# Kernel optimization log

Hardware: AMD Instinct MI355X
Metric: run time of the kernel (lower is better)

The kernel has to match this reference:

```python
import jax, jax.numpy as jnp
import numpy as np

HIDDEN = 300
DEPTH = 3
MAX_NB = 10
AFEAT = 82
BFEAT = 6
B, N, M = 16, 2048, 4096


def setup_inputs() -> dict:
    key = jax.random.key(0)
    ks = jax.random.split(key, 16)
    s = 0.05
    return {
        "input_atom": jax.random.normal(ks[0], (B, N, AFEAT), jnp.float32),
        "input_bond": jax.random.normal(ks[1], (B, M, BFEAT), jnp.float32),
        "node_mask": jnp.ones((B, N, 1), jnp.float32),
        "atom_graph": jax.random.randint(ks[2], (B, N, MAX_NB), 0, N, jnp.int32),
        "bond_graph": jax.random.randint(ks[3], (B, N, MAX_NB), 0, M, jnp.int32),
        "num_nbs": jax.random.randint(ks[4], (B, N), 0, MAX_NB, jnp.int32),
        "W_af": jax.random.normal(ks[5], (AFEAT, HIDDEN), jnp.float32) * s,
        "W_na": jax.random.normal(ks[6], (HIDDEN, HIDDEN), jnp.float32) * s,
        "W_nb": jax.random.normal(ks[7], (BFEAT, HIDDEN), jnp.float32) * s,
        "W_sa": jax.random.normal(ks[8], (HIDDEN, HIDDEN), jnp.float32) * s,
        "W_u2": jax.random.normal(ks[9], (HIDDEN + BFEAT, HIDDEN), jnp.float32) * s,
        "b_u2": jnp.zeros((HIDDEN,), jnp.float32),
        "W_u1": jax.random.normal(ks[10], (2 * HIDDEN, HIDDEN), jnp.float32) * s,
        "b_u1": jnp.zeros((HIDDEN,), jnp.float32),
        "W_out": jax.random.normal(ks[11], (HIDDEN, 1), jnp.float32) * s,
        "b_out": jnp.zeros((1,), jnp.float32),
    }


def _wln(input_atom, input_bond, node_mask, atom_graph, bond_graph, num_nbs,
         W_af, W_na, W_nb, W_sa, W_u2, b_u2, W_u1, b_u1):
    bidx = jnp.arange(input_atom.shape[0])[:, None, None]  # (B,1,1)
    atom_feat = jax.nn.relu(input_atom @ W_af)             # (B,N,H)
    fbond_nei = input_bond[bidx, bond_graph]               # (B,N,max_nb,6) gather
    h_nei_bond = fbond_nei @ W_nb                          # constant over depth
    # neighbor validity mask from num_nbs (sequence mask)
    nb_mask = (jnp.arange(MAX_NB)[None, None, :] < num_nbs[..., None]
               ).astype(atom_feat.dtype)[..., None]        # (B,N,max_nb,1)
    kernel = None
    for _ in range(DEPTH):
        fatom_nei = atom_feat[bidx, atom_graph]            # (B,N,max_nb,H) gather
        h_nei = (fatom_nei @ W_na) * h_nei_bond
        f_nei = jnp.sum(h_nei * nb_mask, axis=-2)          # (B,N,H)
        f_self = atom_feat @ W_sa
        kernel = f_nei * f_self * node_mask                # last-layer WLN kernel
        l_nei = jnp.concatenate([fatom_nei, fbond_nei], axis=-1)
        pre_label = jax.nn.relu(l_nei @ W_u2 + b_u2)
        nei_label = jnp.sum(pre_label * nb_mask, axis=-2)
        new_label = jnp.concatenate([atom_feat, nei_label], axis=-1)
        atom_feat = jax.nn.relu(new_label @ W_u1 + b_u1)
    return kernel


def reference(input_atom, input_bond, node_mask, atom_graph, bond_graph, num_nbs,
              W_af, W_na, W_nb, W_sa, W_u2, b_u2, W_u1, b_u1, W_out, b_out):
    x = _wln(input_atom, input_bond, node_mask, atom_graph, bond_graph, num_nbs,
             W_af, W_na, W_nb, W_sa, W_u2, b_u2, W_u1, b_u1)  # (B,N,H)
    x = jnp.sum(x, axis=-2)                                   # sum pooling -> (B,H)
    return x @ W_out + b_out                                  # (B,1)
```

## Files before the change

kernel.cpp:

```cpp
#include <hip/hip_runtime.h>
#include <math.h>


typedef unsigned short ushort_t;
typedef __attribute__((ext_vector_type(8))) short bf16x8;
typedef __attribute__((ext_vector_type(8))) unsigned short ushort8;
typedef __attribute__((ext_vector_type(4))) float f32x4;

static constexpr int Hh  = 300;
static constexpr int Hp  = 320;
static constexpr int Bn  = 16;
static constexpr int Nn  = 2048;
static constexpr int Rn  = Bn * Nn;
static constexpr int NBn = 10;

static constexpr size_t OFF_U2 = 320 * 96;
static constexpr size_t OFF_NA = OFF_U2 + 320 * 320;
static constexpr size_t OFF_SA = OFF_NA + 320 * 320;
static constexpr size_t OFF_U1 = OFF_SA + 320 * 320;
static constexpr int    W_ELEMS = (int)(OFF_U1 + 320 * 640);

__device__ __forceinline__ ushort_t f2bf(float x) {
    union { float f; unsigned u; } c; c.f = x;
    unsigned r = c.u + 0x7FFFu + ((c.u >> 16) & 1u);
    return (ushort_t)(r >> 16);
}
__device__ __forceinline__ float bf2f(ushort_t h) {
    union { float f; unsigned u; } c; c.u = ((unsigned)h) << 16;
    return c.f;
}

template<bool RELU, bool BIAS, bool CONCAT>
__global__ __launch_bounds__(256)
void mfma_gemm_k(const ushort_t* __restrict__ A, const ushort_t* __restrict__ A2,
                 int lda, int KP,
                 const ushort_t* __restrict__ Wt,
                 const float* __restrict__ bias,
                 ushort_t* __restrict__ C)
{
    __shared__ __attribute__((aligned(16))) ushort_t As[256 * 40];
    __shared__ __attribute__((aligned(16))) ushort_t Bs[64 * 40];

    const int t   = threadIdx.x;
    const int wv  = t >> 6;
    const int ln  = t & 63;
    const int lrow = ln & 15;
    const int lgrp = ln >> 4;
    const int rowBase = blockIdx.y * 256;
    const int nBase   = blockIdx.x * 64;

    f32x4 acc[4][4];
#pragma unroll
    for (int i = 0; i < 4; i++)
#pragma unroll
        for (int j = 0; j < 4; j++) acc[i][j] = (f32x4){0.f, 0.f, 0.f, 0.f};

    const int half = KP >> 1;

    for (int k0 = 0; k0 < KP; k0 += 32) {
#pragma unroll
        for (int e = 0; e < 4; e++) {
            int chunk = t + e * 256;
            int r = chunk >> 2, c = chunk & 3;
            int k = k0 + c * 8;
            const ushort_t* src;
            if (CONCAT && k >= half) src = A2 + (size_t)(rowBase + r) * lda + (k - half);
            else                     src = A  + (size_t)(rowBase + r) * lda + k;
            *(ushort8*)&As[r * 40 + c * 8] = *(const ushort8*)src;
        }
        {
            int r = t >> 2, c = t & 3;
            *(ushort8*)&Bs[r * 40 + c * 8] =
                *(const ushort8*)(Wt + (size_t)(nBase + r) * KP + k0 + c * 8);
        }
        __syncthreads();

        bf16x8 af[4], bfr[4];
#pragma unroll
        for (int mb = 0; mb < 4; mb++)
            af[mb] = *(const bf16x8*)&As[(wv * 64 + mb * 16 + lrow) * 40 + lgrp * 8];
#pragma unroll
        for (int nb = 0; nb < 4; nb++)
            bfr[nb] = *(const bf16x8*)&Bs[(nb * 16 + lrow) * 40 + lgrp * 8];
#pragma unroll
        for (int mb = 0; mb < 4; mb++)
#pragma unroll
            for (int nb = 0; nb < 4; nb++)
                acc[mb][nb] = __builtin_amdgcn_mfma_f32_16x16x32_bf16(
                    af[mb], bfr[nb], acc[mb][nb], 0, 0, 0);
        __syncthreads();
    }

#pragma unroll
    for (int mb = 0; mb < 4; mb++) {
        int row0 = rowBase + wv * 64 + mb * 16 + lgrp * 4;
#pragma unroll
        for (int nb = 0; nb < 4; nb++) {
            int col = nBase + nb * 16 + lrow;
            float bv = 0.f;
            if (BIAS) bv = (col < Hh) ? bias[col] : 0.f;
#pragma unroll
            for (int r = 0; r < 4; r++) {
                float v = acc[mb][nb][r] + bv;
                if (RELU) v = v > 0.f ? v : 0.f;
                C[(size_t)(row0 + r) * Hp + col] = f2bf(v);
            }
        }
    }
}

template<bool FINAL>
__global__ __launch_bounds__(256)
void gather_k(const ushort_t* __restrict__ Arow,
              const ushort_t* __restrict__ Asa,
              const float* __restrict__ bond,
              const float* __restrict__ Wb,
              const float* __restrict__ bias,
              const int*   __restrict__ ag,
              const int*   __restrict__ bg,
              const int*   __restrict__ nnb,
              const float* __restrict__ nmask,
              const float* __restrict__ Wout,
              void* __restrict__ outp)
{
    __shared__ float sWb[6 * Hp];
    __shared__ float sV[Hp];
    __shared__ float sdot[4];
    for (int i = threadIdx.x; i < 6 * Hp; i += 256) {
        int tt = i / Hp, h = i - tt * Hp;
        sWb[i] = (h < Hh) ? Wb[tt * Hh + h] : 0.f;
    }
    for (int i = threadIdx.x; i < Hp; i += 256) {
        float v = 0.f;
        if (i < Hh) v = FINAL ? Wout[i] : bias[i];
        sV[i] = v;
    }
    __syncthreads();

    const int wave = threadIdx.x >> 6;
    const int lane = threadIdx.x & 63;

    int node = blockIdx.x * 4 + wave;

    for (int it = 0; it < 4; it++, node += 2048 * 4) {
        const int b    = node >> 11;
        const int nn   = nnb[node];
        const int base = node * NBn;
        const size_t arow0 = (size_t)(b << 11) * Hp;
        const size_t brow0 = (size_t)(b << 12) * 6;

        const int iav = ag[base + (lane < 10 ? lane : 9)];
        const int ibv = bg[base + (lane < 10 ? lane : 9)];

        float acc[5] = {0.f, 0.f, 0.f, 0.f, 0.f};
        float cA[6], cB[6];
        ushort_t qA[5], qB[5];

        auto issue = [&](int kk, float (&c)[6], ushort_t (&q)[5]) {
            int iak = __shfl(iav, kk);
            int ibk = __shfl(ibv, kk);
            const ushort_t* pa = Arow + arow0 + (size_t)iak * Hp + lane;
            const float*    pf = bond + brow0 + (size_t)ibk * 6;
#pragma unroll
            for (int j = 0; j < 5; j++) q[j] = pa[j * 64];
#pragma unroll
            for (int t2 = 0; t2 < 6; t2++) c[t2] = pf[t2];
        };
        auto consume = [&](const float (&c)[6], const ushort_t (&q)[5]) {
#pragma unroll
            for (int j = 0; j < 5; j++) {
                int h = lane + j * 64;
                float w = c[0] * sWb[h]          + c[1] * sWb[Hp + h]
                        + c[2] * sWb[2 * Hp + h] + c[3] * sWb[3 * Hp + h]
                        + c[4] * sWb[4 * Hp + h] + c[5] * sWb[5 * Hp + h];
                float av = bf2f(q[j]);
                if (FINAL) {
                    acc[j] += av * w;
                } else {
                    float v = av + w + sV[h];
                    acc[j] += v > 0.f ? v : 0.f;
                }
            }
        };

        if (nn > 0) {
            issue(0, cA, qA);
            if (nn > 1) issue(1, cB, qB);
            for (int k = 0; k < nn; k += 2) {
                consume(cA, qA);
                if (k + 2 < nn) issue(k + 2, cA, qA);
                if (k + 1 < nn) {
                    consume(cB, qB);
                    if (k + 3 < nn) issue(k + 3, cB, qB);
                }
            }
        }

        if (FINAL) {
            const ushort_t* psa = Asa + (size_t)node * Hp + lane;
            float dot = 0.f;
#pragma unroll
            for (int j = 0; j < 5; j++) {
                int h = lane + j * 64;
                dot += acc[j] * bf2f(psa[j * 64]) * sV[h];
            }
            dot *= nmask[node];
#pragma unroll
            for (int off = 32; off > 0; off >>= 1) dot += __shfl_down(dot, off, 64);
            if (lane == 0) sdot[wave] = dot;
            __syncthreads();
            if (threadIdx.x == 0)
                atomicAdd(&((float*)outp)[b], sdot[0] + sdot[1] + sdot[2] + sdot[3]);
            __syncthreads();
        } else {
            ushort_t* pl = (ushort_t*)outp + (size_t)node * Hp + lane;
#pragma unroll
            for (int j = 0; j < 5; j++) pl[j * 64] = f2bf(acc[j]);
        }
    }
}

__global__ void zero_k(ushort_t* __restrict__ p, int n)
{
    int i = blockIdx.x * 256 + threadIdx.x;
    if (i < n) p[i] = 0;
}

__global__ void cvt_atom_k(const float* __restrict__ src, ushort_t* __restrict__ dst)
{
    int idx = blockIdx.x * 256 + threadIdx.x;
    if (idx >= Rn * 96) return;
    int r = idx / 96, c = idx - r * 96;
    dst[idx] = (c < 82) ? f2bf(src[r * 82 + c]) : (ushort_t)0;
}

__global__ void cvt_weights_k(const float* __restrict__ W_af,
                              const float* __restrict__ W_u2,
                              const float* __restrict__ W_na,
                              const float* __restrict__ W_sa,
                              const float* __restrict__ W_u1,
                              ushort_t* __restrict__ dst0)
{
    const float* src; int Ksrc, kbase, stride; size_t doff;
    switch (blockIdx.y) {
    case 0:  src = W_af;             Ksrc =  82; kbase = 0;   stride =  96; doff = 0;      break;
    case 1:  src = W_u2;             Ksrc = 300; kbase = 0;   stride = 320; doff = OFF_U2; break;
    case 2:  src = W_na;             Ksrc = 300; kbase = 0;   stride = 320; doff = OFF_NA; break;
    case 3:  src = W_sa;             Ksrc = 300; kbase = 0;   stride = 320; doff = OFF_SA; break;
    case 4:  src = W_u1;             Ksrc = 300; kbase = 0;   stride = 640; doff = OFF_U1; break;
    default: src = W_u1 + 300 * 300; Ksrc = 300; kbase = 320; stride = 640; doff = OFF_U1; break;
    }
    int idx = blockIdx.x * 256 + threadIdx.x;
    if (idx >= Ksrc * Hh) return;
    int k = idx / Hh, n = idx - k * Hh;
    dst0[doff + (size_t)n * stride + kbase + k] = f2bf(src[idx]);
}

__global__ void init_out_k(float* __restrict__ out, const float* __restrict__ b_out)
{
    if (threadIdx.x < Bn) out[threadIdx.x] = b_out[0];
}

extern "C" void kernel_launch(void* const* d_in, const int* in_sizes, int n_in,
                              void* d_out, int out_size, void* d_ws, size_t ws_size,
                              hipStream_t stream)
{
    const float* input_atom = (const float*)d_in[0];
    const float* input_bond = (const float*)d_in[1];
    const float* node_mask  = (const float*)d_in[2];
    const int*   atom_graph = (const int*)d_in[3];
    const int*   bond_graph = (const int*)d_in[4];
    const int*   num_nbs    = (const int*)d_in[5];
    const float* W_af       = (const float*)d_in[6];
    const float* W_na       = (const float*)d_in[7];
    const float* W_nb       = (const float*)d_in[8];
    const float* W_sa       = (const float*)d_in[9];
    const float* W_u2       = (const float*)d_in[10];
    const float* b_u2       = (const float*)d_in[11];
    const float* W_u1       = (const float*)d_in[12];
    const float* b_u1       = (const float*)d_in[13];
    const float* W_out      = (const float*)d_in[14];
    const float* b_out      = (const float*)d_in[15];
    float* out = (float*)d_out;

    const float* W_u2b = W_u2 + (size_t)Hh * Hh;

    const size_t S2 = (size_t)Rn * Hp;
    ushort_t* bufA0 = (ushort_t*)d_ws;
    ushort_t* bufA1 = bufA0 + S2;
    ushort_t* bufP  = bufA1 + S2;
    ushort_t* bufL  = bufP  + S2;
    ushort_t* bufS  = bufL  + S2;
    ushort_t* iaB   = bufS  + S2;
    ushort_t* wAf   = iaB + (size_t)Rn * 96;

    zero_k<<<(W_ELEMS + 255) / 256, 256, 0, stream>>>(wAf, W_ELEMS);
    cvt_atom_k<<<(Rn * 96 + 255) / 256, 256, 0, stream>>>(input_atom, iaB);
    cvt_weights_k<<<dim3(352, 6), 256, 0, stream>>>(W_af, W_u2, W_na, W_sa, W_u1, wAf);
    init_out_k<<<dim3(1), dim3(64), 0, stream>>>(out, b_out);

    dim3 gg(5, Rn / 256);
    const int gb = 2048;

    mfma_gemm_k<true, false, false><<<gg, 256, 0, stream>>>(
        iaB, nullptr, 96, 96, wAf, nullptr, bufA0);

    ushort_t* cur = bufA0;
    ushort_t* oth = bufA1;
    for (int d = 0; d < 2; d++) {
        mfma_gemm_k<false, false, false><<<gg, 256, 0, stream>>>(
            cur, nullptr, Hp, Hp, wAf + OFF_U2, nullptr, bufP);
        gather_k<false><<<gb, 256, 0, stream>>>(
            bufP, nullptr, input_bond, W_u2b, b_u2,
            atom_graph, bond_graph, num_nbs, nullptr, nullptr, bufL);
        mfma_gemm_k<true, true, true><<<gg, 256, 0, stream>>>(
            cur, bufL, Hp, 2 * Hp, wAf + OFF_U1, b_u1, oth);
        ushort_t* tmp = cur; cur = oth; oth = tmp;
    }

    mfma_gemm_k<false, false, false><<<gg, 256, 0, stream>>>(
        cur, nullptr, Hp, Hp, wAf + OFF_NA, nullptr, bufP);
    mfma_gemm_k<false, false, false><<<gg, 256, 0, stream>>>(
        cur, nullptr, Hp, Hp, wAf + OFF_SA, nullptr, bufS);
    gather_k<true><<<gb, 256, 0, stream>>>(
        bufP, bufS, input_bond, W_nb, nullptr,
        atom_graph, bond_graph, num_nbs, node_mask, W_out, out);
}
```

Measured before the change: 491.9 us.

## Stage GEMM and gather loads through LDS with direct global-to-LDS copies

The GEMM tile shrinks from 256 to 128 rows per block and drops the padded LDS layout. Operand tiles are now loaded with global_load_lds direct copies where the builtin is available. The gather kernel now handles one node per wave with more blocks. It batches all neighbor atom rows into LDS through async copies and loads bond features up front, using readfirstlane to make them scalar. The aim is more memory-level parallelism and occupancy, at the cost of possible LDS bank conflicts from the unpadded 32-wide stride and more LDS use per gather block.

Result: slower. 576.1 us (+17.1%).

```diff
diff --git a/kernel.cpp b/kernel.cpp
--- a/kernel.cpp
+++ b/kernel.cpp
@@ -28,6 +28,20 @@
 __device__ __forceinline__ float bf2f(ushort_t h) {
     union { float f; unsigned u; } c; c.u = ((unsigned)h) << 16;
     return c.f;
+}
+
+__device__ __forceinline__ void stage16(const void* g, void* l) {
+#if __has_builtin(__builtin_amdgcn_global_load_lds)
+    __builtin_amdgcn_global_load_lds(
+        (const __attribute__((address_space(1))) void*)g,
+        (__attribute__((address_space(3))) void*)l, 16, 0, 0);
+#else
+    *(ushort8*)l = *(const ushort8*)g;
+#endif
+}
+
+__device__ __forceinline__ float rfl_f(float v) {
+    return __int_as_float(__builtin_amdgcn_readfirstlane(__float_as_int(v)));
 }
 
 template<bool RELU, bool BIAS, bool CONCAT>
@@ -38,20 +52,20 @@
                  const float* __restrict__ bias,
                  ushort_t* __restrict__ C)
 {
-    __shared__ __attribute__((aligned(16))) ushort_t As[256 * 40];
-    __shared__ __attribute__((aligned(16))) ushort_t Bs[64 * 40];
-
-    const int t   = threadIdx.x;
-    const int wv  = t >> 6;
-    const int ln  = t & 63;
+    __shared__ __attribute__((aligned(16))) ushort_t As[128 * 32];
+    __shared__ __attribute__((aligned(16))) ushort_t Bs[64 * 32];
+
+    const int t    = threadIdx.x;
+    const int wv   = t >> 6;
+    const int ln   = t & 63;
     const int lrow = ln & 15;
     const int lgrp = ln >> 4;
-    const int rowBase = blockIdx.y * 256;
+    const int rowBase = blockIdx.y * 128;
     const int nBase   = blockIdx.x * 64;
 
-    f32x4 acc[4][4];
-#pragma unroll
-    for (int i = 0; i < 4; i++)
+    f32x4 acc[2][4];
+#pragma unroll
+    for (int i = 0; i < 2; i++)
 #pragma unroll
         for (int j = 0; j < 4; j++) acc[i][j] = (f32x4){0.f, 0.f, 0.f, 0.f};
 
@@ -59,31 +73,30 @@
 
     for (int k0 = 0; k0 < KP; k0 += 32) {
 #pragma unroll
-        for (int e = 0; e < 4; e++) {
+        for (int e = 0; e < 2; e++) {
             int chunk = t + e * 256;
             int r = chunk >> 2, c = chunk & 3;
             int k = k0 + c * 8;
             const ushort_t* src;
             if (CONCAT && k >= half) src = A2 + (size_t)(rowBase + r) * lda + (k - half);
             else                     src = A  + (size_t)(rowBase + r) * lda + k;
-            *(ushort8*)&As[r * 40 + c * 8] = *(const ushort8*)src;
+            stage16(src, &As[(size_t)chunk * 8]);
         }
         {
             int r = t >> 2, c = t & 3;
-            *(ushort8*)&Bs[r * 40 + c * 8] =
-                *(const ushort8*)(Wt + (size_t)(nBase + r) * KP + k0 + c * 8);
+            stage16(Wt + (size_t)(nBase + r) * KP + k0 + c * 8, &Bs[(size_t)t * 8]);
         }
         __syncthreads();
 
-        bf16x8 af[4], bfr[4];
-#pragma unroll
-        for (int mb = 0; mb < 4; mb++)
-            af[mb] = *(const bf16x8*)&As[(wv * 64 + mb * 16 + lrow) * 40 + lgrp * 8];
+        bf16x8 af[2], bfr[4];
+#pragma unroll
+        for (int mb = 0; mb < 2; mb++)
+            af[mb] = *(const bf16x8*)&As[(wv * 32 + mb * 16 + lrow) * 32 + lgrp * 8];
 #pragma unroll
         for (int nb = 0; nb < 4; nb++)
-            bfr[nb] = *(const bf16x8*)&Bs[(nb * 16 + lrow) * 40 + lgrp * 8];
-#pragma unroll
-        for (int mb = 0; mb < 4; mb++)
+            bfr[nb] = *(const bf16x8*)&Bs[(nb * 16 + lrow) * 32 + lgrp * 8];
+#pragma unroll
+        for (int mb = 0; mb < 2; mb++)
 #pragma unroll
             for (int nb = 0; nb < 4; nb++)
                 acc[mb][nb] = __builtin_amdgcn_mfma_f32_16x16x32_bf16(
@@ -92,8 +105,8 @@
     }
 
 #pragma unroll
-    for (int mb = 0; mb < 4; mb++) {
-        int row0 = rowBase + wv * 64 + mb * 16 + lgrp * 4;
+    for (int mb = 0; mb < 2; mb++) {
+        int row0 = rowBase + wv * 32 + mb * 16 + lgrp * 4;
 #pragma unroll
         for (int nb = 0; nb < 4; nb++) {
             int col = nBase + nb * 16 + lrow;
@@ -125,6 +138,7 @@
 {
     __shared__ float sWb[6 * Hp];
     __shared__ float sV[Hp];
+    __shared__ __attribute__((aligned(16))) ushort_t sAtom[4][NBn][Hp];
     __shared__ float sdot[4];
     for (int i = threadIdx.x; i < 6 * Hp; i += 256) {
         int tt = i / Hp, h = i - tt * Hp;
@@ -139,83 +153,91 @@
 
     const int wave = threadIdx.x >> 6;
     const int lane = threadIdx.x & 63;
-
-    int node = blockIdx.x * 4 + wave;
-
-    for (int it = 0; it < 4; it++, node += 2048 * 4) {
-        const int b    = node >> 11;
-        const int nn   = nnb[node];
-        const int base = node * NBn;
-        const size_t arow0 = (size_t)(b << 11) * Hp;
-        const size_t brow0 = (size_t)(b << 12) * 6;
-
-        const int iav = ag[base + (lane < 10 ? lane : 9)];
-        const int ibv = bg[base + (lane < 10 ? lane : 9)];
-
-        float acc[5] = {0.f, 0.f, 0.f, 0.f, 0.f};
-        float cA[6], cB[6];
-        ushort_t qA[5], qB[5];
-
-        auto issue = [&](int kk, float (&c)[6], ushort_t (&q)[5]) {
-            int iak = __shfl(iav, kk);
-            int ibk = __shfl(ibv, kk);
-            const ushort_t* pa = Arow + arow0 + (size_t)iak * Hp + lane;
-            const float*    pf = bond + brow0 + (size_t)ibk * 6;
-#pragma unroll
-            for (int j = 0; j < 5; j++) q[j] = pa[j * 64];
-#pragma unroll
-            for (int t2 = 0; t2 < 6; t2++) c[t2] = pf[t2];
-        };
-        auto consume = [&](const float (&c)[6], const ushort_t (&q)[5]) {
-#pragma unroll
-            for (int j = 0; j < 5; j++) {
-                int h = lane + j * 64;
-                float w = c[0] * sWb[h]          + c[1] * sWb[Hp + h]
-                        + c[2] * sWb[2 * Hp + h] + c[3] * sWb[3 * Hp + h]
-                        + c[4] * sWb[4 * Hp + h] + c[5] * sWb[5 * Hp + h];
-                float av = bf2f(q[j]);
+    const int node = blockIdx.x * 4 + wave;
+    const int b    = node >> 11;
+    const int nn   = nnb[node];
+    const int base = node * NBn;
+    const size_t arow0 = (size_t)(b << 11) * Hp;
+    const size_t brow0 = (size_t)(b << 12) * 6;
+
+    const int iav = ag[base + (lane < 10 ? lane : 9)];
+    const int ibv = bg[base + (lane < 10 ? lane : 9)];
+
+    float tmpc[NBn][6];
+#pragma unroll
+    for (int k = 0; k < NBn; k++) {
+        if (k < nn) {
+            int ibk = __shfl(ibv, k);
+            const float* pf = bond + brow0 + (size_t)ibk * 6;
+#pragma unroll
+            for (int tt = 0; tt < 6; tt++) tmpc[k][tt] = pf[tt];
+        }
+    }
+#pragma unroll
+    for (int k = 0; k < NBn; k++) {
+        if (k < nn) {
+            int iak = __shfl(iav, k);
+            const ushort_t* pa = Arow + arow0 + (size_t)iak * Hp;
+            if (lane < 40)
+                stage16(pa + (size_t)lane * 8, &sAtom[wave][k][lane * 8]);
+        }
+    }
+    float c[NBn][6];
+#pragma unroll
+    for (int k = 0; k < NBn; k++) {
+        if (k < nn) {
+#pragma unroll
+            for (int tt = 0; tt < 6; tt++) c[k][tt] = rfl_f(tmpc[k][tt]);
+        }
+    }
+    asm volatile("s_waitcnt vmcnt(0)" ::: "memory");
+
+    float acc[5];
+#pragma unroll
+    for (int j = 0; j < 5; j++) {
+        const int h = lane + j * 64;
+        const float w0 = sWb[h],          w1 = sWb[Hp + h],     w2 = sWb[2 * Hp + h];
+        const float w3 = sWb[3 * Hp + h], w4 = sWb[4 * Hp + h], w5 = sWb[5 * Hp + h];
+        const float sv = FINAL ? 0.f : sV[h];
+        float a = 0.f;
+#pragma unroll
+        for (int k = 0; k < NBn; k++) {
+            if (k < nn) {
+                float av = bf2f(sAtom[wave][k][h]);
+                float w  = c[k][0] * w0 + c[k][1] * w1 + c[k][2] * w2
+                         + c[k][3] * w3 + c[k][4] * w4 + c[k][5] * w5;
                 if (FINAL) {
-                    acc[j] += av * w;
+                    a += av * w;
                 } else {
-                    float v = av + w + sV[h];
-                    acc[j] += v > 0.f ? v : 0.f;
+                    float v = av + w + sv;
+                    a += v > 0.f ? v : 0.f;
                 }
             }
-        };
-
-        if (nn > 0) {
-            issue(0, cA, qA);
-            if (nn > 1) issue(1, cB, qB);
-            for (int k = 0; k < nn; k += 2) {
-                consume(cA, qA);
-                if (k + 2 < nn) issue(k + 2, cA, qA);
-                if (k + 1 < nn) {
-                    consume(cB, qB);
-                    if (k + 3 < nn) issue(k + 3, cB, qB);
-                }
-            }
-        }
-
-        if (FINAL) {
-            const ushort_t* psa = Asa + (size_t)node * Hp + lane;
-            float dot = 0.f;
-#pragma unroll
-            for (int j = 0; j < 5; j++) {
-                int h = lane + j * 64;
-                dot += acc[j] * bf2f(psa[j * 64]) * sV[h];
-            }
-            dot *= nmask[node];
-#pragma unroll
-            for (int off = 32; off > 0; off >>= 1) dot += __shfl_down(dot, off, 64);
-            if (lane == 0) sdot[wave] = dot;
-            __syncthreads();
-            if (threadIdx.x == 0)
-                atomicAdd(&((float*)outp)[b], sdot[0] + sdot[1] + sdot[2] + sdot[3]);
-            __syncthreads();
-        } else {
-            ushort_t* pl = (ushort_t*)outp + (size_t)node * Hp + lane;
-#pragma unroll
-            for (int j = 0; j < 5; j++) pl[j * 64] = f2bf(acc[j]);
+        }
+        acc[j] = a;
+    }
+
+    if (FINAL) {
+        const ushort_t* psa = Asa + (size_t)node * Hp + lane;
+        float dot = 0.f;
+#pragma unroll
+        for (int j = 0; j < 5; j++) {
+            int h = lane + j * 64;
+            dot += acc[j] * bf2f(psa[j * 64]) * sV[h];
+        }
+        dot *= nmask[node];
+#pragma unroll
+        for (int off = 32; off > 0; off >>= 1) dot += __shfl_down(dot, off, 64);
+        if (lane == 0) sdot[wave] = dot;
+        __syncthreads();
+        if (threadIdx.x == 0)
+            atomicAdd(&((float*)outp)[b], sdot[0] + sdot[1] + sdot[2] + sdot[3]);
+    } else {
+        ushort_t* pl = (ushort_t*)outp + (size_t)node * Hp + lane;
+#pragma unroll
+        for (int j = 0; j < 5; j++) {
+            int h = lane + j * 64;
+            pl[j * 64] = (h < Hh) ? f2bf(acc[j]) : (ushort_t)0;
         }
     }
 }
@@ -299,8 +321,8 @@
     cvt_weights_k<<<dim3(352, 6), 256, 0, stream>>>(W_af, W_u2, W_na, W_sa, W_u1, wAf);
     init_out_k<<<dim3(1), dim3(64), 0, stream>>>(out, b_out);
 
-    dim3 gg(5, Rn / 256);
-    const int gb = 2048;
+    dim3 gg(5, Rn / 128);
+    const int gb = Rn / 4;
 
     mfma_gemm_k<true, false, false><<<gg, 256, 0, stream>>>(
         iaB, nullptr, 96, 96, wAf, nullptr, bufA0);
```
